# Performance work log

Measured on AMD Instinct MI355X. Metric: run time of the kernel, lower is better.

The kernel has to match this reference:

```python
import jax, jax.numpy as jnp
import numpy as np

B, S, D = 32, 2048, 512
NUM_SEG = 65  # mask//100 in [0, 64]; segment 0 is padding, dropped from output


def setup_inputs() -> dict:
    key = jax.random.key(0)
    k1, k2 = jax.random.split(key)
    output = jax.random.normal(k1, (B, S, D), dtype=jnp.float32)
    mask = jax.random.randint(k2, (B, S), 0, 6500, dtype=jnp.int64)
    return {"output": output, "mask": mask}


def reference(output, mask):
    # torch_scatter.scatter_mean(src=output, index=mask//100, dim=-2)[:, 1:, :]
    seg = mask // 100  # [B, S] segment ids in [0, NUM_SEG)
    sums = jax.vmap(
        lambda o, s: jax.ops.segment_sum(o, s, num_segments=NUM_SEG)
    )(output, seg)  # [B, NUM_SEG, D]
    counts = jax.vmap(
        lambda s: jax.ops.segment_sum(
            jnp.ones(s.shape, dtype=output.dtype), s, num_segments=NUM_SEG
        )
    )(seg)  # [B, NUM_SEG]
    # scatter_mean yields 0 for empty segments; clamping count to 1 preserves that
    mean = sums / jnp.maximum(counts, 1.0)[..., None]
    return mean[:, 1:, :]  # drop segment 0 (padding), -> [B, NUM_SEG-1, D]
```

## Files before the change

### kernel.cpp

```cpp
#include <hip/hip_runtime.h>


constexpr int S = 2048;
constexpr int D = 512;
constexpr int D4 = D / 4;
constexpr int NSEG_OUT = 64;

__global__ __launch_bounds__(256, 8) void seg_mean_kernel(
    const float* __restrict__ src,
    const int* __restrict__ mask,
    float* __restrict__ dst) {
  const int segm1 = blockIdx.x;
  const int b = blockIdx.y;
  const int tid = threadIdx.x;
  const int w = tid >> 6;
  const int lane = tid & 63;
  const int myseg = segm1 + 1;

  __shared__ float sums[4][D];
  __shared__ short list[4][512];
  __shared__ int wcnt[4];

  const int4* m4 = (const int4*)(mask + (size_t)b * S) + (size_t)w * 128;
  const int4 q0 = m4[lane];
  const int4 q1 = m4[64 + lane];

  unsigned long long bal[8];
  bal[0] = __ballot(q0.x / 100 == myseg);
  bal[1] = __ballot(q0.y / 100 == myseg);
  bal[2] = __ballot(q0.z / 100 == myseg);
  bal[3] = __ballot(q0.w / 100 == myseg);
  bal[4] = __ballot(q1.x / 100 == myseg);
  bal[5] = __ballot(q1.y / 100 == myseg);
  bal[6] = __ballot(q1.z / 100 == myseg);
  bal[7] = __ballot(q1.w / 100 == myseg);

  int cnt = 0;
  #pragma unroll
  for (int r = 0; r < 8; ++r) {
    unsigned long long bb = bal[r];
    const int sb = 512 * w + 256 * (r >> 2) + (r & 3);
    while (bb) {
      const int L = __ffsll((long long)bb) - 1;
      bb &= bb - 1;
      if (lane == 0) list[w][cnt] = (short)(sb + 4 * L);
      ++cnt;
    }
  }
  if (lane == 0) wcnt[w] = cnt;

  const float4* row4 = (const float4*)(src + (size_t)b * S * D);
  float4 a0 = make_float4(0.f, 0.f, 0.f, 0.f);
  float4 a1 = make_float4(0.f, 0.f, 0.f, 0.f);

  int i = 0;
  for (; i + 1 < cnt; i += 2) {
    const int s0 = list[w][i];
    const int s1 = list[w][i + 1];
    const float4* r0 = row4 + (size_t)s0 * D4;
    const float4* r1 = row4 + (size_t)s1 * D4;
    const float4 v00 = r0[lane];
    const float4 v01 = r0[64 + lane];
    const float4 v10 = r1[lane];
    const float4 v11 = r1[64 + lane];
    a0.x += v00.x; a0.y += v00.y; a0.z += v00.z; a0.w += v00.w;
    a1.x += v01.x; a1.y += v01.y; a1.z += v01.z; a1.w += v01.w;
    a0.x += v10.x; a0.y += v10.y; a0.z += v10.z; a0.w += v10.w;
    a1.x += v11.x; a1.y += v11.y; a1.z += v11.z; a1.w += v11.w;
  }
  if (i < cnt) {
    const int s0 = list[w][i];
    const float4* r0 = row4 + (size_t)s0 * D4;
    const float4 v00 = r0[lane];
    const float4 v01 = r0[64 + lane];
    a0.x += v00.x; a0.y += v00.y; a0.z += v00.z; a0.w += v00.w;
    a1.x += v01.x; a1.y += v01.y; a1.z += v01.z; a1.w += v01.w;
  }

  ((float4*)sums[w])[lane] = a0;
  ((float4*)sums[w])[64 + lane] = a1;
  __syncthreads();

  if (tid < D4) {
    const int m = wcnt[0] + wcnt[1] + wcnt[2] + wcnt[3];
    const float inv = 1.0f / fmaxf((float)m, 1.0f);
    const float4 s0 = ((const float4*)sums[0])[tid];
    const float4 s1 = ((const float4*)sums[1])[tid];
    const float4 s2 = ((const float4*)sums[2])[tid];
    const float4 s3 = ((const float4*)sums[3])[tid];
    float4 r;
    r.x = (s0.x + s1.x + s2.x + s3.x) * inv;
    r.y = (s0.y + s1.y + s2.y + s3.y) * inv;
    r.z = (s0.z + s1.z + s2.z + s3.z) * inv;
    r.w = (s0.w + s1.w + s2.w + s3.w) * inv;
    float4* out4 = (float4*)(dst + ((size_t)b * NSEG_OUT + segm1) * D);
    out4[tid] = r;
  }
}

extern "C" void kernel_launch(void* const* d_in, const int* in_sizes, int n_in,
                              void* d_out, int out_size, void* d_ws, size_t ws_size,
                              hipStream_t stream) {
  const float* src = (const float*)d_in[0];
  const int* mask = (const int*)d_in[1];
  float* dst = (float*)d_out;

  dim3 grid(NSEG_OUT, 32);
  seg_mean_kernel<<<grid, 256, 0, stream>>>(src, mask, dst);
}
```

Before: 27.61 us.

## Build shared segment row list with parallel prefix scan and balance rows across waves

Each wave now computes its matching-row offsets with popcount prefix sums, and every lane writes its own entry into one block-wide shared list, replacing the serial ffs loop where only lane 0 wrote. The combined list is then split evenly across the four waves, so imbalance between waves' row counts no longer lengthens the block. The gather loop is unrolled to four rows to keep more loads in flight. It costs an extra block barrier and more registers in the unrolled loop.

```diff
diff --git a/kernel.cpp b/kernel.cpp
--- a/kernel.cpp
+++ b/kernel.cpp
@@ -18,7 +18,7 @@
   const int myseg = segm1 + 1;
 
   __shared__ float sums[4][D];
-  __shared__ short list[4][512];
+  __shared__ short list[S];
   __shared__ int wcnt[4];
 
   const int4* m4 = (const int4*)(mask + (size_t)b * S) + (size_t)w * 128;
@@ -35,44 +35,60 @@
   bal[6] = __ballot(q1.z / 100 == myseg);
   bal[7] = __ballot(q1.w / 100 == myseg);
 
+  int pre[8];
   int cnt = 0;
   #pragma unroll
+  for (int r = 0; r < 8; ++r) { pre[r] = cnt; cnt += __popcll(bal[r]); }
+  if (lane == 0) wcnt[w] = cnt;
+  __syncthreads();
+
+  const int c0 = wcnt[0], c1 = wcnt[1], c2 = wcnt[2], c3 = wcnt[3];
+  const int m = c0 + c1 + c2 + c3;
+  int base = 0;
+  if (w > 0) base += c0;
+  if (w > 1) base += c1;
+  if (w > 2) base += c2;
+
+  const unsigned long long mylow = (1ull << lane) - 1ull;
+  #pragma unroll
   for (int r = 0; r < 8; ++r) {
-    unsigned long long bb = bal[r];
-    const int sb = 512 * w + 256 * (r >> 2) + (r & 3);
-    while (bb) {
-      const int L = __ffsll((long long)bb) - 1;
-      bb &= bb - 1;
-      if (lane == 0) list[w][cnt] = (short)(sb + 4 * L);
-      ++cnt;
+    if ((bal[r] >> lane) & 1ull) {
+      const int pos = pre[r] + __popcll(bal[r] & mylow);
+      list[base + pos] = (short)(512 * w + 256 * (r >> 2) + 4 * lane + (r & 3));
     }
   }
-  if (lane == 0) wcnt[w] = cnt;
+  __syncthreads();
 
+  const int lo = (m * w) >> 2;
+  const int hi = (m * (w + 1)) >> 2;
   const float4* row4 = (const float4*)(src + (size_t)b * S * D);
   float4 a0 = make_float4(0.f, 0.f, 0.f, 0.f);
   float4 a1 = make_float4(0.f, 0.f, 0.f, 0.f);
 
-  int i = 0;
-  for (; i + 1 < cnt; i += 2) {
-    const int s0 = list[w][i];
-    const int s1 = list[w][i + 1];
+  int i = lo;
+  for (; i + 3 < hi; i += 4) {
+    const int s0 = list[i], s1 = list[i + 1], s2 = list[i + 2], s3 = list[i + 3];
     const float4* r0 = row4 + (size_t)s0 * D4;
     const float4* r1 = row4 + (size_t)s1 * D4;
-    const float4 v00 = r0[lane];
-    const float4 v01 = r0[64 + lane];
-    const float4 v10 = r1[lane];
-    const float4 v11 = r1[64 + lane];
+    const float4* r2 = row4 + (size_t)s2 * D4;
+    const float4* r3 = row4 + (size_t)s3 * D4;
+    const float4 v00 = r0[lane],      v01 = r0[64 + lane];
+    const float4 v10 = r1[lane],      v11 = r1[64 + lane];
+    const float4 v20 = r2[lane],      v21 = r2[64 + lane];
+    const float4 v30 = r3[lane],      v31 = r3[64 + lane];
     a0.x += v00.x; a0.y += v00.y; a0.z += v00.z; a0.w += v00.w;
     a1.x += v01.x; a1.y += v01.y; a1.z += v01.z; a1.w += v01.w;
     a0.x += v10.x; a0.y += v10.y; a0.z += v10.z; a0.w += v10.w;
     a1.x += v11.x; a1.y += v11.y; a1.z += v11.z; a1.w += v11.w;
+    a0.x += v20.x; a0.y += v20.y; a0.z += v20.z; a0.w += v20.w;
+    a1.x += v21.x; a1.y += v21.y; a1.z += v21.z; a1.w += v21.w;
+    a0.x += v30.x; a0.y += v30.y; a0.z += v30.z; a0.w += v30.w;
+    a1.x += v31.x; a1.y += v31.y; a1.z += v31.z; a1.w += v31.w;
   }
-  if (i < cnt) {
-    const int s0 = list[w][i];
+  for (; i < hi; ++i) {
+    const int s0 = list[i];
     const float4* r0 = row4 + (size_t)s0 * D4;
-    const float4 v00 = r0[lane];
-    const float4 v01 = r0[64 + lane];
+    const float4 v00 = r0[lane], v01 = r0[64 + lane];
     a0.x += v00.x; a0.y += v00.y; a0.z += v00.z; a0.w += v00.w;
     a1.x += v01.x; a1.y += v01.y; a1.z += v01.z; a1.w += v01.w;
   }
@@ -82,7 +98,6 @@
   __syncthreads();
 
   if (tid < D4) {
-    const int m = wcnt[0] + wcnt[1] + wcnt[2] + wcnt[3];
     const float inv = 1.0f / fmaxf((float)m, 1.0f);
     const float4 s0 = ((const float4*)sums[0])[tid];
     const float4 s1 = ((const float4*)sums[1])[tid];
```

New measurement: 26.79 us. -3.0%, faster.
